# Performance work log

Hardware: AMD Instinct MI355X
Metric: run time of the kernel (lower is better)

## Reference

```python
import jax, jax.numpy as jnp
import numpy as np

D_MODEL, D_HIDDEN = 1024, 2048
B, L = 4, 4096


def setup_inputs() -> dict:
    key = jax.random.key(0)
    ks = jax.random.split(key, 16)
    r = lambda k, shape, s: s * jax.random.normal(k, shape, dtype=jnp.float32)
    inp = {
        "x": r(ks[0], (B, L, D_MODEL), 1.0),
        # MambaBlock weights (torch Linear stores [out, in]; bias=False for these)
        "w1": r(ks[1], (D_MODEL, D_MODEL), 0.02),
        "w2": r(ks[2], (D_MODEL, D_MODEL), 0.02),
        "w3": r(ks[3], (D_MODEL, D_MODEL), 0.02),
        # depthwise Conv1d: weight [D, 1, 3], bias [D]
        "conv_w": r(ks[4], (D_MODEL, 1, 3), 0.1),
        "conv_b": r(ks[5], (D_MODEL,), 0.02),
        # SSM linears (with bias). Scales keep exp(-delta*A) in (0,1) and
        # the length-L cumprod away from fp32 underflow.
        "A_w": r(ks[6], (D_HIDDEN, D_MODEL), 0.001),
        "A_b": jnp.ones((D_HIDDEN,), jnp.float32),
        "B_w": r(ks[7], (D_HIDDEN, D_MODEL), 0.02),
        "B_b": jnp.zeros((D_HIDDEN,), jnp.float32),
        "C_w": r(ks[8], (D_MODEL, D_HIDDEN), 0.02),
        "C_b": jnp.zeros((D_MODEL,), jnp.float32),
        "D_w": r(ks[9], (D_MODEL, D_MODEL), 0.02),
        "D_b": jnp.zeros((D_MODEL,), jnp.float32),
        "dl_w": r(ks[10], (D_HIDDEN, D_MODEL), 0.001),
        "dl_b": -5.0 * jnp.ones((D_HIDDEN,), jnp.float32),
    }
    return inp


def _lin(x, w, b=None):
    y = jnp.einsum("bld,od->blo", x, w)
    return y if b is None else y + b


def _depthwise_conv(x, conv_w, conv_b):
    # x: [B, L, D] -> torch Conv1d(D, D, k=3, pad=1, groups=D) on [B, D, L]
    lhs = jnp.transpose(x, (0, 2, 1))  # [B, D, L]
    y = jax.lax.conv_general_dilated(
        lhs, conv_w, window_strides=(1,), padding=[(1, 1)],
        dimension_numbers=("NCH", "OIH", "NCH"), feature_group_count=D_MODEL)
    y = y + conv_b[None, :, None]
    return jnp.transpose(y, (0, 2, 1))  # [B, L, D]


def reference(x, w1, w2, w3, conv_w, conv_b, A_w, A_b, B_w, B_b,
              C_w, C_b, D_w, D_b, dl_w, dl_b):
    x = _lin(x, w1)                              # linear1 (no bias)
    x = _depthwise_conv(x, conv_w, conv_b)       # depthwise conv1d
    x = jax.nn.silu(x)
    # SSM
    x_delta = jax.nn.softplus(_lin(x, dl_w, dl_b))   # [B, L, H]
    A_t = _lin(x, A_w, A_b)                          # [B, L, H]
    A_bar = jnp.exp(-x_delta * A_t)                  # [B, L, H]
    B_x = _lin(x, B_w, B_b)                          # [B, L, H]
    A_cum = jnp.cumprod(A_bar, axis=1)               # scan over seq
    h = jnp.cumsum(B_x * A_cum, axis=1)
    ssm_out = _lin(h, C_w, C_b) + _lin(x, D_w, D_b)  # [B, L, D]
    # gated output
    x_res = jax.nn.silu(_lin(ssm_out, w2))
    z = ssm_out * x_res
    out = ssm_out + _lin(z, w3)
    return out
```

## Files before the change

### kernel.cpp

```cpp
#include <hip/hip_runtime.h>
#include <hip/hip_bf16.h>
#include <stdint.h>
#include <math.h>

#define DM 1024
#define DH 2048
#define NB 4
#define SL 4096
#define MT (NB*SL)
#define LC 256
#define NC (SL/LC)

typedef __bf16 bf16;
typedef __attribute__((ext_vector_type(8))) __bf16 bf16x8;
typedef __attribute__((ext_vector_type(4))) __bf16 bf16x4;
typedef __attribute__((ext_vector_type(4))) float f32x4;

__global__ void cvt_kernel(const float* __restrict__ in, bf16* __restrict__ out, int n) {
  const int n4 = n >> 2;
  for (int i = blockIdx.x * 256 + threadIdx.x; i < n4; i += gridDim.x * 256) {
    f32x4 v = *(const f32x4*)(in + 4 * (size_t)i);
    bf16x4 o;
#pragma unroll
    for (int j = 0; j < 4; ++j) {
      float x = v[j];
      x = (x == x) ? fminf(fmaxf(x, -65504.f), 65504.f) : 0.f;
      o[j] = (bf16)x;
    }
    *(bf16x4*)(out + 4 * (size_t)i) = o;
  }
}

template<int MODE, bool HAS_BIAS, int N, int K>
__global__ __launch_bounds__(256, 3)
void gemm_bt(const bf16* __restrict__ A, const bf16* __restrict__ W,
             const float* __restrict__ bias, const void* __restrict__ extra,
             void* __restrict__ outp) {
  __shared__ __align__(16) char pool[34816];
  bf16* lds_a = (bf16*)pool;
  bf16* lds_b = (bf16*)(pool + 16384);

  const int tid  = threadIdx.x;
  const int wave = tid >> 6;
  const int lane = tid & 63;
  const int wm = wave >> 1, wn = wave & 1;

  constexpr int NBN = N / 128;
  const int nbm8 = (int)(gridDim.y >> 3);
  const int id   = (int)(blockIdx.y * NBN + blockIdx.x);
  const int xcd  = id & 7;
  const unsigned jj = (unsigned)id >> 3;
  const int bm   = xcd * nbm8 + (int)(jj / (unsigned)NBN);
  const int bn   = (int)(jj & (NBN - 1));

  const int r_in = lane >> 3;
  const int kc_l = (lane & 7) ^ r_in;
  const size_t arow0 = (size_t)bm * 128;
  const size_t brow0 = (size_t)bn * 128;

  f32x4 acc[4][4];
#pragma unroll
  for (int i = 0; i < 4; ++i)
#pragma unroll
    for (int j = 0; j < 4; ++j) acc[i][j] = {0.f, 0.f, 0.f, 0.f};

  const int mrow = lane & 15;
  const int kg   = lane >> 4;

  const bf16* pa[4];
  const bf16* pb[4];
#pragma unroll
  for (int iss = 0; iss < 4; ++iss) {
    const int chunk = iss * 4 + wave;
    const int row   = chunk * 8 + r_in;
    pa[iss] = A + (arow0 + row) * (size_t)K + kc_l * 8;
    pb[iss] = W + (brow0 + row) * (size_t)K + kc_l * 8;
  }

  bf16x8 va[4], vb[4];
#pragma unroll
  for (int iss = 0; iss < 4; ++iss) {
    va[iss] = *(const bf16x8*)pa[iss]; pa[iss] += 64;
    vb[iss] = *(const bf16x8*)pb[iss]; pb[iss] += 64;
  }

#pragma unroll 1
  for (int k0 = 0; k0 < K; k0 += 64) {
    __syncthreads();
#pragma unroll
    for (int iss = 0; iss < 4; ++iss) {
      const int chunk = iss * 4 + wave;
      *(bf16x8*)&lds_a[chunk * 512 + lane * 8] = va[iss];
      *(bf16x8*)&lds_b[chunk * 512 + lane * 8] = vb[iss];
    }
    __syncthreads();
    if (k0 + 64 < K) {
#pragma unroll
      for (int iss = 0; iss < 4; ++iss) {
        va[iss] = *(const bf16x8*)pa[iss]; pa[iss] += 64;
        vb[iss] = *(const bf16x8*)pb[iss]; pb[iss] += 64;
      }
    }
#pragma unroll
    for (int ks = 0; ks < 2; ++ks) {
      bf16x8 af[4], bfr[4];
#pragma unroll
      for (int t = 0; t < 4; ++t) {
        const int ra = wm * 64 + t * 16 + mrow;
        const int sa = ra * 8 + ((ks * 4 + kg) ^ (ra & 7));
        af[t] = *(const bf16x8*)&lds_a[sa * 8];
        const int rb = wn * 64 + t * 16 + mrow;
        const int sb = rb * 8 + ((ks * 4 + kg) ^ (rb & 7));
        bfr[t] = *(const bf16x8*)&lds_b[sb * 8];
      }
#pragma unroll
      for (int i = 0; i < 4; ++i)
#pragma unroll
        for (int j = 0; j < 4; ++j)
          acc[i][j] = __builtin_amdgcn_mfma_f32_16x16x32_bf16(af[i], bfr[j], acc[i][j], 0, 0, 0);
    }
  }

  __syncthreads();
  float* eps = (float*)pool + wave * 2176;
  const int rr  = lane >> 3;
  const int cc  = (lane & 7) * 8;
  const int gcol0 = bn * 128 + wn * 64 + cc;
  f32x4 bv0 = {0.f, 0.f, 0.f, 0.f}, bv1 = {0.f, 0.f, 0.f, 0.f};
  if constexpr (HAS_BIAS) {
    bv0 = *(const f32x4*)(bias + gcol0);
    bv1 = *(const f32x4*)(bias + gcol0 + 4);
  }

#pragma unroll
  for (int p = 0; p < 2; ++p) {
#pragma unroll
    for (int ii = 0; ii < 2; ++ii) {
      const int i = p * 2 + ii;
#pragma unroll
      for (int j = 0; j < 4; ++j) {
#pragma unroll
        for (int r = 0; r < 4; ++r) {
          const int lr = ii * 16 + kg * 4 + r;
          eps[lr * 68 + j * 16 + mrow] = acc[i][j][r];
        }
      }
    }
#pragma unroll
    for (int rnd = 0; rnd < 4; ++rnd) {
      const int lr   = rnd * 8 + rr;
      const int grow = bm * 128 + wm * 64 + p * 32 + lr;
      f32x4 v0 = *(const f32x4*)&eps[lr * 68 + cc];
      f32x4 v1 = *(const f32x4*)&eps[lr * 68 + cc + 4];
      const size_t off = (size_t)grow * N + gcol0;
      float vv[8];
#pragma unroll
      for (int k = 0; k < 4; ++k) { vv[k] = v0[k] + bv0[k]; vv[4 + k] = v1[k] + bv1[k]; }

      float res[8];
      if constexpr (MODE == 0 || MODE == 1) {
#pragma unroll
        for (int k = 0; k < 8; ++k) res[k] = vv[k];
      } else if constexpr (MODE == 2) {
        f32x4 e0 = *(const f32x4*)((const float*)extra + off);
        f32x4 e1 = *(const f32x4*)((const float*)extra + off + 4);
#pragma unroll
        for (int k = 0; k < 4; ++k) { res[k] = vv[k] + e0[k]; res[4 + k] = vv[4 + k] + e1[k]; }
      } else if constexpr (MODE == 3) {
        bf16x8 g = *(const bf16x8*)((const bf16*)extra + off);
#pragma unroll
        for (int k = 0; k < 8; ++k) {
          const float v = vv[k];
          res[k] = (float)g[k] * (v / (1.f + __expf(-v)));
        }
      } else if constexpr (MODE == 4) {
        bf16x8 e = *(const bf16x8*)((const bf16*)extra + off);
#pragma unroll
        for (int k = 0; k < 8; ++k) res[k] = vv[k] + (float)e[k];
      } else if constexpr (MODE == 5) {
#pragma unroll
        for (int k = 0; k < 8; ++k) {
          const float v = vv[k];
          res[k] = (v > 15.f) ? v : __logf(1.f + __expf(v));
        }
      } else {
        bf16x8 d = *(const bf16x8*)((const bf16*)extra + off);
#pragma unroll
        for (int k = 0; k < 8; ++k) res[k] = (float)d[k] * vv[k];
      }

      if constexpr (MODE == 1 || MODE == 4) {
        f32x4 o0, o1;
#pragma unroll
        for (int k = 0; k < 4; ++k) { o0[k] = res[k]; o1[k] = res[4 + k]; }
        *(f32x4*)((float*)outp + off)     = o0;
        *(f32x4*)((float*)outp + off + 4) = o1;
      } else {
        bf16x8 o;
#pragma unroll
        for (int k = 0; k < 8; ++k) o[k] = (bf16)res[k];
        *(bf16x8*)((bf16*)outp + off) = o;
      }
    }
  }
}

__global__ void conv_silu_kernel(const bf16* __restrict__ t1, const float* __restrict__ cw,
                                 const float* __restrict__ cb, bf16* __restrict__ xc) {
  const int gid  = blockIdx.x * 256 + threadIdx.x;
  const int dgrp = gid & (DM / 8 - 1);
  const int bl   = gid >> 7;
  const int l    = bl & (SL - 1);
  const int d0   = dgrp * 8;
  const bf16* p  = t1 + (size_t)bl * DM + d0;
  bf16x8 cc = *(const bf16x8*)p;
  bf16x8 lf, rt;
#pragma unroll
  for (int j = 0; j < 8; ++j) { lf[j] = (bf16)0.f; rt[j] = (bf16)0.f; }
  if (l > 0)      lf = *(const bf16x8*)(p - DM);
  if (l < SL - 1) rt = *(const bf16x8*)(p + DM);
  bf16x8 o;
#pragma unroll
  for (int j = 0; j < 8; ++j) {
    const int d = d0 + j;
    float y = cw[d * 3 + 0] * (float)lf[j] + cw[d * 3 + 1] * (float)cc[j]
            + cw[d * 3 + 2] * (float)rt[j] + cb[d];
    y = y / (1.f + __expf(-y));
    o[j] = (bf16)y;
  }
  *(bf16x8*)(xc + (size_t)bl * DM + d0) = o;
}

__global__ void scan_phase1(bf16* nla_sl, const bf16* __restrict__ bx,
                            float* __restrict__ Lp_tot, float* __restrict__ T_tot) {
  const int g  = blockIdx.x * 256 + threadIdx.x;
  const int ch = g & (DH - 1);
  const int rc = g >> 11;
  const int b  = rc & (NB - 1);
  const int c  = rc >> 2;
  const int bc = b * DH + ch;
  size_t off = ((size_t)(b * SL + c * LC)) * DH + ch;
  float lp = 0.f, S = 0.f;
#pragma unroll 8
  for (int l = 0; l < LC; ++l, off += DH) {
    const float a = (float)nla_sl[off];
    const float x = (float)bx[off];
    lp += a;
    const float e = __expf(-fminf(fmaxf(lp, -80.f), 80.f));
    S = fmaf(x, e, S);
    nla_sl[off] = (bf16)S;
  }
  Lp_tot[c * (NB * DH) + bc] = lp;
  T_tot [c * (NB * DH) + bc] = S;
}

__global__ void scan_phase2(const float* __restrict__ Lp_tot, const float* __restrict__ T_tot,
                            float* __restrict__ lpoff, float* __restrict__ Soff) {
  const int bc = blockIdx.x * 256 + threadIdx.x;
  float lp = 0.f, S = 0.f;
#pragma unroll
  for (int c = 0; c < NC; ++c) {
    lpoff[c * (NB * DH) + bc] = lp;
    Soff [c * (NB * DH) + bc] = S;
    const float e = __expf(-fminf(fmaxf(lp, -80.f), 80.f));
    S  = fmaf(e, T_tot[c * (NB * DH) + bc], S);
    lp += Lp_tot[c * (NB * DH) + bc];
  }
}

__global__ void scan_phase3(const bf16* __restrict__ S_local, bf16* __restrict__ h,
                            const float* __restrict__ lpoff, const float* __restrict__ Soff) {
  const int g  = blockIdx.x * 256 + threadIdx.x;
  const int ch = g & (DH - 1);
  const int rc = g >> 11;
  const int b  = rc & (NB - 1);
  const int c  = rc >> 2;
  const int bc = b * DH + ch;
  const float lo = lpoff[c * (NB * DH) + bc];
  const float so = Soff [c * (NB * DH) + bc];
  const float es = __expf(-fminf(fmaxf(lo, -80.f), 80.f));
  size_t off = ((size_t)(b * SL + c * LC)) * DH + ch;
#pragma unroll 8
  for (int l = 0; l < LC; ++l, off += DH) {
    h[off] = (bf16)fmaf(es, (float)S_local[off], so);
  }
}

extern "C" void kernel_launch(void* const* d_in, const int* in_sizes, int n_in,
                              void* d_out, int out_size, void* d_ws, size_t ws_size,
                              hipStream_t stream) {
  const float* x    = (const float*)d_in[0];
  const float* w1   = (const float*)d_in[1];
  const float* w2   = (const float*)d_in[2];
  const float* w3   = (const float*)d_in[3];
  const float* cw   = (const float*)d_in[4];
  const float* cb   = (const float*)d_in[5];
  const float* A_w  = (const float*)d_in[6];
  const float* A_b  = (const float*)d_in[7];
  const float* B_w  = (const float*)d_in[8];
  const float* B_b  = (const float*)d_in[9];
  const float* C_w  = (const float*)d_in[10];
  const float* C_b  = (const float*)d_in[11];
  const float* D_w  = (const float*)d_in[12];
  const float* D_b  = (const float*)d_in[13];
  const float* dl_w = (const float*)d_in[14];
  const float* dl_b = (const float*)d_in[15];

  const size_t MB = 1048576u;
  char* ws = (char*)d_ws;
  bf16* w1b  = (bf16*)(ws + 0*MB);
  bf16* w2b  = (bf16*)(ws + 2*MB);
  bf16* w3b  = (bf16*)(ws + 4*MB);
  bf16* Dwb  = (bf16*)(ws + 6*MB);
  bf16* Awb  = (bf16*)(ws + 8*MB);
  bf16* Bwb  = (bf16*)(ws + 12*MB);
  bf16* dlwb = (bf16*)(ws + 16*MB);
  bf16* Cwb  = (bf16*)(ws + 20*MB);
  bf16* xc   = (bf16*)(ws + 24*MB);
  bf16* ssm  = xc;
  bf16* t1   = (bf16*)(ws + 56*MB);
  bf16* z    = t1;
  bf16* xbf  = (bf16*)(ws + 88*MB);
  bf16* dlo  = (bf16*)(ws + 56*MB);
  bf16* bxh  = dlo;
  bf16* nla  = (bf16*)(ws + 120*MB);
  float* dtmp = (float*)nla;
  float* Lp_tot = (float*)(ws + 184*MB);
  float* T_tot  = (float*)(ws + 184*MB + 524288u);
  float* lpoff  = (float*)(ws + 185*MB);
  float* Soff   = (float*)(ws + 185*MB + 524288u);
  float* outp = (float*)d_out;

  dim3 blk(256);
  dim3 g1(DM / 128, MT / 128);
  dim3 g2(DH / 128, MT / 128);

  cvt_kernel<<<4096, blk, 0, stream>>>(x,    xbf,  MT*DM);
  cvt_kernel<<<512,  blk, 0, stream>>>(w1,   w1b,  DM*DM);
  cvt_kernel<<<512,  blk, 0, stream>>>(w2,   w2b,  DM*DM);
  cvt_kernel<<<512,  blk, 0, stream>>>(w3,   w3b,  DM*DM);
  cvt_kernel<<<512,  blk, 0, stream>>>(D_w,  Dwb,  DM*DM);
  cvt_kernel<<<1024, blk, 0, stream>>>(A_w,  Awb,  DH*DM);
  cvt_kernel<<<1024, blk, 0, stream>>>(B_w,  Bwb,  DH*DM);
  cvt_kernel<<<1024, blk, 0, stream>>>(dl_w, dlwb, DH*DM);
  cvt_kernel<<<1024, blk, 0, stream>>>(C_w,  Cwb,  DM*DH);

  gemm_bt<0,false,DM,DM><<<g1, blk, 0, stream>>>(xbf, w1b,  nullptr, nullptr, t1);
  conv_silu_kernel<<<MT * DM / 8 / 256, blk, 0, stream>>>(t1, cw, cb, xc);
  gemm_bt<5,true ,DH,DM><<<g2, blk, 0, stream>>>(xc,  dlwb, dl_b,    nullptr, dlo);
  gemm_bt<6,true ,DH,DM><<<g2, blk, 0, stream>>>(xc,  Awb,  A_b,     dlo,     nla);
  gemm_bt<0,true ,DH,DM><<<g2, blk, 0, stream>>>(xc,  Bwb,  B_b,     nullptr, bxh);
  scan_phase1<<<MT * NC * DH / SL / 256, blk, 0, stream>>>(nla, bxh, Lp_tot, T_tot);
  scan_phase2<<<NB * DH / 256, blk, 0, stream>>>(Lp_tot, T_tot, lpoff, Soff);
  scan_phase3<<<MT * NC * DH / SL / 256, blk, 0, stream>>>(nla, bxh, lpoff, Soff);
  gemm_bt<1,true ,DM,DM><<<g1, blk, 0, stream>>>(xc,  Dwb,  D_b,     nullptr, dtmp);
  gemm_bt<2,true ,DM,DH><<<g1, blk, 0, stream>>>(bxh, Cwb,  C_b,     dtmp,    ssm);
  gemm_bt<3,false,DM,DM><<<g1, blk, 0, stream>>>(ssm, w2b,  nullptr, ssm,     z);
  gemm_bt<4,false,DM,DM><<<g1, blk, 0, stream>>>(z,   w3b,  nullptr, ssm,     outp);
}
```

Baseline: 743.5 us.

## Fuse delta/A GEMMs and C/D GEMMs, load tiles via direct global-to-LDS

The delta and A projections, which share the same input, are merged into one dual-accumulator GEMM that applies softplus(delta)*A in its epilogue, so the input tile is read once and the bf16 delta intermediate disappears. The C and D projections become a single GEMM that accumulates two K passes into the same accumulators, which removes the fp32 dtmp buffer and its round trip. Tile loads switch from register staging to global_load_lds. This drops the previous register-level prefetch, so loads are no longer overlapped with MFMA work and each K step now sits behind the barrier. The dual kernel also uses more LDS and registers, which lowers occupancy to 2 blocks.

```diff
diff --git a/kernel.cpp b/kernel.cpp
--- a/kernel.cpp
+++ b/kernel.cpp
@@ -31,39 +31,23 @@
   }
 }
 
-template<int MODE, bool HAS_BIAS, int N, int K>
-__global__ __launch_bounds__(256, 3)
-void gemm_bt(const bf16* __restrict__ A, const bf16* __restrict__ W,
-             const float* __restrict__ bias, const void* __restrict__ extra,
-             void* __restrict__ outp) {
-  __shared__ __align__(16) char pool[34816];
-  bf16* lds_a = (bf16*)pool;
-  bf16* lds_b = (bf16*)(pool + 16384);
-
-  const int tid  = threadIdx.x;
-  const int wave = tid >> 6;
-  const int lane = tid & 63;
+
+__device__ __forceinline__ void g2lds(const bf16* g, bf16* l) {
+  __builtin_amdgcn_global_load_lds((const __attribute__((address_space(1))) void*)g,
+                                   (__attribute__((address_space(3))) void*)l,
+                                   16, 0, 0);
+}
+
+template<int KK>
+__device__ __forceinline__ void gemm_pass(const bf16* __restrict__ Abase,
+                                          const bf16* __restrict__ Wbase,
+                                          bf16* lds_a, bf16* lds_b,
+                                          f32x4 (&acc)[4][4],
+                                          int wave, int lane,
+                                          size_t arow0, size_t brow0) {
   const int wm = wave >> 1, wn = wave & 1;
-
-  constexpr int NBN = N / 128;
-  const int nbm8 = (int)(gridDim.y >> 3);
-  const int id   = (int)(blockIdx.y * NBN + blockIdx.x);
-  const int xcd  = id & 7;
-  const unsigned jj = (unsigned)id >> 3;
-  const int bm   = xcd * nbm8 + (int)(jj / (unsigned)NBN);
-  const int bn   = (int)(jj & (NBN - 1));
-
   const int r_in = lane >> 3;
   const int kc_l = (lane & 7) ^ r_in;
-  const size_t arow0 = (size_t)bm * 128;
-  const size_t brow0 = (size_t)bn * 128;
-
-  f32x4 acc[4][4];
-#pragma unroll
-  for (int i = 0; i < 4; ++i)
-#pragma unroll
-    for (int j = 0; j < 4; ++j) acc[i][j] = {0.f, 0.f, 0.f, 0.f};
-
   const int mrow = lane & 15;
   const int kg   = lane >> 4;
 
@@ -71,36 +55,21 @@
   const bf16* pb[4];
 #pragma unroll
   for (int iss = 0; iss < 4; ++iss) {
-    const int chunk = iss * 4 + wave;
-    const int row   = chunk * 8 + r_in;
-    pa[iss] = A + (arow0 + row) * (size_t)K + kc_l * 8;
-    pb[iss] = W + (brow0 + row) * (size_t)K + kc_l * 8;
-  }
-
-  bf16x8 va[4], vb[4];
-#pragma unroll
-  for (int iss = 0; iss < 4; ++iss) {
-    va[iss] = *(const bf16x8*)pa[iss]; pa[iss] += 64;
-    vb[iss] = *(const bf16x8*)pb[iss]; pb[iss] += 64;
+    const int row = (iss * 4 + wave) * 8 + r_in;
+    pa[iss] = Abase + (arow0 + row) * (size_t)KK + kc_l * 8;
+    pb[iss] = Wbase + (brow0 + row) * (size_t)KK + kc_l * 8;
   }
 
 #pragma unroll 1
-  for (int k0 = 0; k0 < K; k0 += 64) {
+  for (int k0 = 0; k0 < KK; k0 += 64) {
     __syncthreads();
 #pragma unroll
     for (int iss = 0; iss < 4; ++iss) {
       const int chunk = iss * 4 + wave;
-      *(bf16x8*)&lds_a[chunk * 512 + lane * 8] = va[iss];
-      *(bf16x8*)&lds_b[chunk * 512 + lane * 8] = vb[iss];
+      g2lds(pa[iss], &lds_a[chunk * 512]); pa[iss] += 64;
+      g2lds(pb[iss], &lds_b[chunk * 512]); pb[iss] += 64;
     }
     __syncthreads();
-    if (k0 + 64 < K) {
-#pragma unroll
-      for (int iss = 0; iss < 4; ++iss) {
-        va[iss] = *(const bf16x8*)pa[iss]; pa[iss] += 64;
-        vb[iss] = *(const bf16x8*)pb[iss]; pb[iss] += 64;
-      }
-    }
 #pragma unroll
     for (int ks = 0; ks < 2; ++ks) {
       bf16x8 af[4], bfr[4];
@@ -120,6 +89,46 @@
           acc[i][j] = __builtin_amdgcn_mfma_f32_16x16x32_bf16(af[i], bfr[j], acc[i][j], 0, 0, 0);
     }
   }
+}
+
+template<int MODE, bool HAS_BIAS, int N, int K1, int K2>
+__global__ __launch_bounds__(256, 3)
+void gemm_bt(const bf16* __restrict__ A1, const bf16* __restrict__ W1,
+             const float* __restrict__ bias1,
+             const bf16* __restrict__ A2, const bf16* __restrict__ W2,
+             const float* __restrict__ bias2,
+             const void* __restrict__ extra, void* __restrict__ outp) {
+  __shared__ __align__(16) char pool[34816];
+  bf16* lds_a = (bf16*)pool;
+  bf16* lds_b = (bf16*)(pool + 16384);
+
+  const int tid  = threadIdx.x;
+  const int wave = tid >> 6;
+  const int lane = tid & 63;
+  const int wm = wave >> 1, wn = wave & 1;
+
+  constexpr int NBN = N / 128;
+  const int nbm8 = (int)(gridDim.y >> 3);
+  const int id   = (int)(blockIdx.y * NBN + blockIdx.x);
+  const int xcd  = id & 7;
+  const unsigned jj = (unsigned)id >> 3;
+  const int bm   = xcd * nbm8 + (int)(jj / (unsigned)NBN);
+  const int bn   = (int)(jj & (NBN - 1));
+  const size_t arow0 = (size_t)bm * 128;
+  const size_t brow0 = (size_t)bn * 128;
+
+  f32x4 acc[4][4];
+#pragma unroll
+  for (int i = 0; i < 4; ++i)
+#pragma unroll
+    for (int j = 0; j < 4; ++j) acc[i][j] = {0.f, 0.f, 0.f, 0.f};
+
+  gemm_pass<K1>(A1, W1, lds_a, lds_b, acc, wave, lane, arow0, brow0);
+  if constexpr (K2 > 0)
+    gemm_pass<K2>(A2, W2, lds_a, lds_b, acc, wave, lane, arow0, brow0);
+
+  const int mrow = lane & 15;
+  const int kg   = lane >> 4;
 
   __syncthreads();
   float* eps = (float*)pool + wave * 2176;
@@ -128,8 +137,12 @@
   const int gcol0 = bn * 128 + wn * 64 + cc;
   f32x4 bv0 = {0.f, 0.f, 0.f, 0.f}, bv1 = {0.f, 0.f, 0.f, 0.f};
   if constexpr (HAS_BIAS) {
-    bv0 = *(const f32x4*)(bias + gcol0);
-    bv1 = *(const f32x4*)(bias + gcol0 + 4);
+    bv0 = *(const f32x4*)(bias1 + gcol0);
+    bv1 = *(const f32x4*)(bias1 + gcol0 + 4);
+  }
+  if constexpr (K2 > 0) {
+    bv0 += *(const f32x4*)(bias2 + gcol0);
+    bv1 += *(const f32x4*)(bias2 + gcol0 + 4);
   }
 
 #pragma unroll
@@ -138,13 +151,10 @@
     for (int ii = 0; ii < 2; ++ii) {
       const int i = p * 2 + ii;
 #pragma unroll
-      for (int j = 0; j < 4; ++j) {
-#pragma unroll
-        for (int r = 0; r < 4; ++r) {
-          const int lr = ii * 16 + kg * 4 + r;
-          eps[lr * 68 + j * 16 + mrow] = acc[i][j][r];
-        }
-      }
+      for (int j = 0; j < 4; ++j)
+#pragma unroll
+        for (int r = 0; r < 4; ++r)
+          eps[(ii * 16 + kg * 4 + r) * 68 + j * 16 + mrow] = acc[i][j][r];
     }
 #pragma unroll
     for (int rnd = 0; rnd < 4; ++rnd) {
@@ -158,38 +168,23 @@
       for (int k = 0; k < 4; ++k) { vv[k] = v0[k] + bv0[k]; vv[4 + k] = v1[k] + bv1[k]; }
 
       float res[8];
-      if constexpr (MODE == 0 || MODE == 1) {
+      if constexpr (MODE == 0) {
 #pragma unroll
         for (int k = 0; k < 8; ++k) res[k] = vv[k];
-      } else if constexpr (MODE == 2) {
-        f32x4 e0 = *(const f32x4*)((const float*)extra + off);
-        f32x4 e1 = *(const f32x4*)((const float*)extra + off + 4);
-#pragma unroll
-        for (int k = 0; k < 4; ++k) { res[k] = vv[k] + e0[k]; res[4 + k] = vv[4 + k] + e1[k]; }
-      } else if constexpr (MODE == 3) {
+      } else if constexpr (MODE == 1) {
+        bf16x8 e = *(const bf16x8*)((const bf16*)extra + off);
+#pragma unroll
+        for (int k = 0; k < 8; ++k) res[k] = vv[k] + (float)e[k];
+      } else {
         bf16x8 g = *(const bf16x8*)((const bf16*)extra + off);
 #pragma unroll
         for (int k = 0; k < 8; ++k) {
           const float v = vv[k];
           res[k] = (float)g[k] * (v / (1.f + __expf(-v)));
         }
-      } else if constexpr (MODE == 4) {
-        bf16x8 e = *(const bf16x8*)((const bf16*)extra + off);
-#pragma unroll
-        for (int k = 0; k < 8; ++k) res[k] = vv[k] + (float)e[k];
-      } else if constexpr (MODE == 5) {
-#pragma unroll
-        for (int k = 0; k < 8; ++k) {
-          const float v = vv[k];
-          res[k] = (v > 15.f) ? v : __logf(1.f + __expf(v));
-        }
-      } else {
-        bf16x8 d = *(const bf16x8*)((const bf16*)extra + off);
-#pragma unroll
-        for (int k = 0; k < 8; ++k) res[k] = (float)d[k] * vv[k];
       }
 
-      if constexpr (MODE == 1 || MODE == 4) {
+      if constexpr (MODE == 1) {
         f32x4 o0, o1;
 #pragma unroll
         for (int k = 0; k < 4; ++k) { o0[k] = res[k]; o1[k] = res[4 + k]; }
@@ -201,6 +196,132 @@
         for (int k = 0; k < 8; ++k) o[k] = (bf16)res[k];
         *(bf16x8*)((bf16*)outp + off) = o;
       }
+    }
+  }
+}
+
+template<int N, int K>
+__global__ __launch_bounds__(256, 2)
+void gemm_dual(const bf16* __restrict__ A, const bf16* __restrict__ W1,
+               const bf16* __restrict__ W2, const float* __restrict__ b1,
+               const float* __restrict__ b2, bf16* __restrict__ outp) {
+  __shared__ __align__(16) char pool[69632];
+  bf16* lds_a  = (bf16*)pool;
+  bf16* lds_b1 = (bf16*)(pool + 16384);
+  bf16* lds_b2 = (bf16*)(pool + 32768);
+
+  const int tid  = threadIdx.x;
+  const int wave = tid >> 6;
+  const int lane = tid & 63;
+  const int wm = wave >> 1, wn = wave & 1;
+
+  constexpr int NBN = N / 128;
+  const int nbm8 = (int)(gridDim.y >> 3);
+  const int id   = (int)(blockIdx.y * NBN + blockIdx.x);
+  const int xcd  = id & 7;
+  const unsigned jj = (unsigned)id >> 3;
+  const int bm   = xcd * nbm8 + (int)(jj / (unsigned)NBN);
+  const int bn   = (int)(jj & (NBN - 1));
+  const size_t arow0 = (size_t)bm * 128;
+  const size_t brow0 = (size_t)bn * 128;
+
+  const int r_in = lane >> 3;
+  const int kc_l = (lane & 7) ^ r_in;
+  const int mrow = lane & 15;
+  const int kg   = lane >> 4;
+
+  f32x4 acc1[4][4], acc2[4][4];
+#pragma unroll
+  for (int i = 0; i < 4; ++i)
+#pragma unroll
+    for (int j = 0; j < 4; ++j) { acc1[i][j] = {0.f,0.f,0.f,0.f}; acc2[i][j] = {0.f,0.f,0.f,0.f}; }
+
+  const bf16* pa[4]; const bf16* pb1[4]; const bf16* pb2[4];
+#pragma unroll
+  for (int iss = 0; iss < 4; ++iss) {
+    const int row = (iss * 4 + wave) * 8 + r_in;
+    pa[iss]  = A  + (arow0 + row) * (size_t)K + kc_l * 8;
+    pb1[iss] = W1 + (brow0 + row) * (size_t)K + kc_l * 8;
+    pb2[iss] = W2 + (brow0 + row) * (size_t)K + kc_l * 8;
+  }
+
+#pragma unroll 1
+  for (int k0 = 0; k0 < K; k0 += 64) {
+    __syncthreads();
+#pragma unroll
+    for (int iss = 0; iss < 4; ++iss) {
+      const int chunk = iss * 4 + wave;
+      g2lds(pa[iss],  &lds_a [chunk * 512]); pa[iss]  += 64;
+      g2lds(pb1[iss], &lds_b1[chunk * 512]); pb1[iss] += 64;
+      g2lds(pb2[iss], &lds_b2[chunk * 512]); pb2[iss] += 64;
+    }
+    __syncthreads();
+#pragma unroll
+    for (int ks = 0; ks < 2; ++ks) {
+      bf16x8 af[4], b1f[4], b2f[4];
+#pragma unroll
+      for (int t = 0; t < 4; ++t) {
+        const int ra = wm * 64 + t * 16 + mrow;
+        const int sa = ra * 8 + ((ks * 4 + kg) ^ (ra & 7));
+        af[t] = *(const bf16x8*)&lds_a[sa * 8];
+        const int rb = wn * 64 + t * 16 + mrow;
+        const int sb = rb * 8 + ((ks * 4 + kg) ^ (rb & 7));
+        b1f[t] = *(const bf16x8*)&lds_b1[sb * 8];
+        b2f[t] = *(const bf16x8*)&lds_b2[sb * 8];
+      }
+#pragma unroll
+      for (int i = 0; i < 4; ++i)
+#pragma unroll
+        for (int j = 0; j < 4; ++j) {
+          acc1[i][j] = __builtin_amdgcn_mfma_f32_16x16x32_bf16(af[i], b1f[j], acc1[i][j], 0, 0, 0);
+          acc2[i][j] = __builtin_amdgcn_mfma_f32_16x16x32_bf16(af[i], b2f[j], acc2[i][j], 0, 0, 0);
+        }
+    }
+  }
+
+  __syncthreads();
+  float* eps1 = (float*)pool + wave * 4352;
+  float* eps2 = eps1 + 2176;
+  const int rr  = lane >> 3;
+  const int cc  = (lane & 7) * 8;
+  const int gcol0 = bn * 128 + wn * 64 + cc;
+  f32x4 b1v0 = *(const f32x4*)(b1 + gcol0);
+  f32x4 b1v1 = *(const f32x4*)(b1 + gcol0 + 4);
+  f32x4 b2v0 = *(const f32x4*)(b2 + gcol0);
+  f32x4 b2v1 = *(const f32x4*)(b2 + gcol0 + 4);
+
+#pragma unroll
+  for (int p = 0; p < 2; ++p) {
+#pragma unroll
+    for (int ii = 0; ii < 2; ++ii) {
+      const int i = p * 2 + ii;
+#pragma unroll
+      for (int j = 0; j < 4; ++j)
+#pragma unroll
+        for (int r = 0; r < 4; ++r) {
+          const int lr = ii * 16 + kg * 4 + r;
+          eps1[lr * 68 + j * 16 + mrow] = acc1[i][j][r];
+          eps2[lr * 68 + j * 16 + mrow] = acc2[i][j][r];
+        }
+    }
+#pragma unroll
+    for (int rnd = 0; rnd < 4; ++rnd) {
+      const int lr   = rnd * 8 + rr;
+      const int grow = bm * 128 + wm * 64 + p * 32 + lr;
+      f32x4 u0 = *(const f32x4*)&eps1[lr * 68 + cc];
+      f32x4 u1 = *(const f32x4*)&eps1[lr * 68 + cc + 4];
+      f32x4 w0 = *(const f32x4*)&eps2[lr * 68 + cc];
+      f32x4 w1v = *(const f32x4*)&eps2[lr * 68 + cc + 4];
+      const size_t off = (size_t)grow * N + gcol0;
+      bf16x8 o;
+#pragma unroll
+      for (int k = 0; k < 8; ++k) {
+        const float dv = (k < 4 ? u0[k] + b1v0[k] : u1[k - 4] + b1v1[k - 4]);
+        const float av = (k < 4 ? w0[k] + b2v0[k] : w1v[k - 4] + b2v1[k - 4]);
+        const float sp = (dv > 15.f) ? dv : __logf(1.f + __expf(dv));
+        o[k] = (bf16)(sp * av);
+      }
+      *(bf16x8*)(outp + off) = o;
     }
   }
 }
@@ -317,14 +438,12 @@
   bf16* dlwb = (bf16*)(ws + 16*MB);
   bf16* Cwb  = (bf16*)(ws + 20*MB);
   bf16* xc   = (bf16*)(ws + 24*MB);
-  bf16* ssm  = xc;
   bf16* t1   = (bf16*)(ws + 56*MB);
   bf16* z    = t1;
   bf16* xbf  = (bf16*)(ws + 88*MB);
-  bf16* dlo  = (bf16*)(ws + 56*MB);
-  bf16* bxh  = dlo;
+  bf16* bxh  = (bf16*)(ws + 56*MB);
   bf16* nla  = (bf16*)(ws + 120*MB);
-  float* dtmp = (float*)nla;
+  bf16* ssm  = (bf16*)(ws + 120*MB);
   float* Lp_tot = (float*)(ws + 184*MB);
   float* T_tot  = (float*)(ws + 184*MB + 524288u);
   float* lpoff  = (float*)(ws + 185*MB);
@@ -345,16 +464,19 @@
   cvt_kernel<<<1024, blk, 0, stream>>>(dl_w, dlwb, DH*DM);
   cvt_kernel<<<1024, blk, 0, stream>>>(C_w,  Cwb,  DM*DH);
 
-  gemm_bt<0,false,DM,DM><<<g1, blk, 0, stream>>>(xbf, w1b,  nullptr, nullptr, t1);
+  gemm_bt<0,false,DM,DM,0><<<g1, blk, 0, stream>>>(xbf, w1b, nullptr,
+      nullptr, nullptr, nullptr, nullptr, t1);
   conv_silu_kernel<<<MT * DM / 8 / 256, blk, 0, stream>>>(t1, cw, cb, xc);
-  gemm_bt<5,true ,DH,DM><<<g2, blk, 0, stream>>>(xc,  dlwb, dl_b,    nullptr, dlo);
-  gemm_bt<6,true ,DH,DM><<<g2, blk, 0, stream>>>(xc,  Awb,  A_b,     dlo,     nla);
-  gemm_bt<0,true ,DH,DM><<<g2, blk, 0, stream>>>(xc,  Bwb,  B_b,     nullptr, bxh);
+  gemm_dual<DH,DM><<<g2, blk, 0, stream>>>(xc, dlwb, Awb, dl_b, A_b, nla);
+  gemm_bt<0,true ,DH,DM,0><<<g2, blk, 0, stream>>>(xc, Bwb, B_b,
+      nullptr, nullptr, nullptr, nullptr, bxh);
   scan_phase1<<<MT * NC * DH / SL / 256, blk, 0, stream>>>(nla, bxh, Lp_tot, T_tot);
   scan_phase2<<<NB * DH / 256, blk, 0, stream>>>(Lp_tot, T_tot, lpoff, Soff);
   scan_phase3<<<MT * NC * DH / SL / 256, blk, 0, stream>>>(nla, bxh, lpoff, Soff);
-  gemm_bt<1,true ,DM,DM><<<g1, blk, 0, stream>>>(xc,  Dwb,  D_b,     nullptr, dtmp);
-  gemm_bt<2,true ,DM,DH><<<g1, blk, 0, stream>>>(bxh, Cwb,  C_b,     dtmp,    ssm);
-  gemm_bt<3,false,DM,DM><<<g1, blk, 0, stream>>>(ssm, w2b,  nullptr, ssm,     z);
-  gemm_bt<4,false,DM,DM><<<g1, blk, 0, stream>>>(z,   w3b,  nullptr, ssm,     outp);
-}
+  gemm_bt<0,true ,DM,DH,DM><<<g1, blk, 0, stream>>>(bxh, Cwb, C_b,
+      xc, Dwb, D_b, nullptr, ssm);
+  gemm_bt<2,false,DM,DM,0><<<g1, blk, 0, stream>>>(ssm, w2b, nullptr,
+      nullptr, nullptr, nullptr, ssm, z);
+  gemm_bt<1,false,DM,DM,0><<<g1, blk, 0, stream>>>(z,   w3b, nullptr,
+      nullptr, nullptr, nullptr, ssm, outp);
+}
```

Result: faster. 661.1 us (-11.1%).
